# Kernel tuning notes

Hardware: AMD Instinct MI355X
Metric: run time of the kernel (lower is better)

## Reference

```python
import jax, jax.numpy as jnp
import numpy as np
import math

D_MODEL = 1024
NUM_HEADS = 16
HEAD_DIM = D_MODEL // NUM_HEADS
THETA = 10000.0
B, S = 2, 2048


def apply_rope(x, pos, theta=THETA):
    # x: [..., S, D]; pos: [S] int. Rotates consecutive (even, odd) pairs.
    d = x.shape[-1]
    inv_freq = theta ** (-jnp.arange(0, d, 2, dtype=jnp.float32) / d)  # [d/2]
    ang = pos.astype(jnp.float32)[:, None] * inv_freq[None, :]          # [S, d/2]
    cos, sin = jnp.cos(ang), jnp.sin(ang)
    xe = x[..., 0::2]
    xo = x[..., 1::2]
    re = xe * cos - xo * sin
    ro = xe * sin + xo * cos
    return jnp.stack([re, ro], axis=-1).reshape(x.shape)


def setup_inputs() -> dict:
    key = jax.random.key(0)
    ks = jax.random.split(key, 5)
    scale = 1.0 / math.sqrt(D_MODEL)
    return {
        "in_features": jax.random.normal(ks[0], (B, S, D_MODEL), dtype=jnp.float32),
        "token_positions": jnp.arange(S, dtype=jnp.int32),
        "wq": jax.random.normal(ks[1], (D_MODEL, D_MODEL), dtype=jnp.float32) * scale,
        "wk": jax.random.normal(ks[2], (D_MODEL, D_MODEL), dtype=jnp.float32) * scale,
        "wv": jax.random.normal(ks[3], (D_MODEL, D_MODEL), dtype=jnp.float32) * scale,
        "wo": jax.random.normal(ks[4], (D_MODEL, D_MODEL), dtype=jnp.float32) * scale,
    }


def reference(in_features, token_positions, wq, wk, wv, wo):
    x = in_features
    b, s, d = x.shape
    # Linear: y = x @ W.T  (weight stored as [out, in])
    def split_heads(y):
        return y.reshape(b, s, NUM_HEADS, HEAD_DIM).transpose(0, 2, 1, 3)  # [B,H,S,Dh]
    Q = split_heads(x @ wq.T)
    K = split_heads(x @ wk.T)
    V = split_heads(x @ wv.T)
    Q = apply_rope(Q, token_positions)
    K = apply_rope(K, token_positions)
    scores = jnp.einsum('bhqd,bhkd->bhqk', Q, K) / math.sqrt(HEAD_DIM)
    causal = jnp.tril(jnp.ones((s, s), dtype=bool))
    scores = jnp.where(causal, scores, -jnp.inf)
    weights = jax.nn.softmax(scores, axis=-1)
    out = jnp.einsum('bhqk,bhkd->bhqd', weights, V)  # [B,H,S,Dh]
    out = out.transpose(0, 2, 1, 3).reshape(b, s, d)
    return out @ wo.T
```

## Files before the change

kernel.cpp:

```cpp
#include <hip/hip_runtime.h>
#include <hip/hip_bf16.h>

typedef __bf16 bf16_t;
typedef __bf16 bf16x8 __attribute__((ext_vector_type(8)));
typedef __bf16 bf16x4 __attribute__((ext_vector_type(4)));
typedef float  f32x4  __attribute__((ext_vector_type(4)));
typedef float  f32x16 __attribute__((ext_vector_type(16)));
typedef unsigned int u32;
typedef unsigned int u32x2v __attribute__((ext_vector_type(2)));
typedef unsigned int u32x4v __attribute__((ext_vector_type(4)));

#define D_MODEL   1024
#define NQKV      3072
#define NUM_HEADS 16
#define HEAD_DIM  64
#define SEQ       2048
#define BATCH     2
#define NTOK      4096
#define SM_SCALE_LOG2E 0.18033688011112042f
#define NEG_BIG  (-3.0e38f)

__device__ __forceinline__ int swz128(int row, int bytecol) {
  return row*128 + ((((bytecol>>4) ^ (row&7))<<4) | (bytecol & 15));
}

__device__ __forceinline__ void gload16(const void* g, void* l) {
  __builtin_amdgcn_global_load_lds((const __attribute__((address_space(1))) u32*)g,
                                   (__attribute__((address_space(3))) u32*)l, 16, 0, 0);
}

__device__ __forceinline__ u32 cvtpk_bf16(float a, float b) {
  u32 r;
  asm("v_cvt_pk_bf16_f32 %0, %1, %2" : "=v"(r) : "v"(a), "v"(b));
  return r;
}

__device__ __forceinline__ void plswap(u32 &a, u32 &b) {
#if __has_builtin(__builtin_amdgcn_permlane32_swap)
  u32x2v r = __builtin_amdgcn_permlane32_swap(a, b, false, false);
  a = r[0]; b = r[1];
#else
  u32 xa = __shfl_xor((unsigned)a, 32, 64);
  u32 xb = __shfl_xor((unsigned)b, 32, 64);
  bool hi = (threadIdx.x & 32) != 0;
  a = hi ? xb : a;
  b = hi ? b : xa;
#endif
}

__device__ const unsigned char slot_order96[96] = {
  30,31,88,90,92,93,94,95,
  28,29,80,82,84,85,86,87,89,91,
  26,27,72,74,76,77,78,79,81,83,
  24,25,64,66,68,69,70,71,73,75,
  22,23,56,58,60,61,62,63,65,67,
  20,21,48,50,52,53,54,55,57,59,
  18,19,40,42,44,45,46,47,49,51,
  16,17,32,34,36,37,38,39,41,43,
  14,15,33,35,
  12,13, 10,11, 8,9, 6,7, 4,5, 2,3, 0,1
};

__global__ void cvt_x(const float* __restrict__ in, bf16_t* __restrict__ out) {
  int i = (blockIdx.x*256 + threadIdx.x)*4;
  float4 v = *reinterpret_cast<const float4*>(in + i);
  bf16x4 o; o[0]=(bf16_t)v.x; o[1]=(bf16_t)v.y; o[2]=(bf16_t)v.z; o[3]=(bf16_t)v.w;
  *reinterpret_cast<bf16x4*>(out + i) = o;
}

__global__ void cvt_w(const float* __restrict__ wq, const float* __restrict__ wk,
                      const float* __restrict__ wv, const float* __restrict__ wo,
                      bf16_t* __restrict__ wqkv, bf16_t* __restrict__ wob) {
  const int NW = D_MODEL*D_MODEL;
  int i = (blockIdx.x*256 + threadIdx.x)*4;
  float4 v;
  if      (i <   NW) v = *reinterpret_cast<const float4*>(wq + i);
  else if (i < 2*NW) v = *reinterpret_cast<const float4*>(wk + i - NW);
  else if (i < 3*NW) v = *reinterpret_cast<const float4*>(wv + i - 2*NW);
  else               v = *reinterpret_cast<const float4*>(wo + i - 3*NW);
  bf16x4 o; o[0]=(bf16_t)v.x; o[1]=(bf16_t)v.y; o[2]=(bf16_t)v.z; o[3]=(bf16_t)v.w;
  bf16_t* dst = (i < 3*NW) ? (wqkv + i) : (wob + i - 3*NW);
  *reinterpret_cast<bf16x4*>(dst) = o;
}

__global__ void rope_qk(bf16_t* __restrict__ QKV, const int* __restrict__ pos) {
  int i = blockIdx.x*256 + threadIdx.x;
  int j = i & 31;
  int hp = (i >> 5) & 15;
  int t  = i >> 9;
  float ang = (float)pos[t & (SEQ-1)] * exp2f(-(float)j * (13.287712379549449f/32.0f));
  float sv, cv; sincosf(ang, &sv, &cv);
  size_t base = (size_t)t*NQKV + hp*64 + 2*j;
  float xe = (float)QKV[base], xo = (float)QKV[base+1];
  QKV[base]   = (bf16_t)((xe*cv - xo*sv)*SM_SCALE_LOG2E);
  QKV[base+1] = (bf16_t)((xe*sv + xo*cv)*SM_SCALE_LOG2E);
  xe = (float)QKV[base+1024]; xo = (float)QKV[base+1025];
  QKV[base+1024] = (bf16_t)(xe*cv - xo*sv);
  QKV[base+1025] = (bf16_t)(xe*sv + xo*cv);
}

template<typename OutT, bool QKV>
__global__ __launch_bounds__(256, 1) void gemm8(const bf16_t* __restrict__ A,
                                                const bf16_t* __restrict__ B,
                                                OutT* __restrict__ C,
                                                bf16_t* __restrict__ Vt,
                                                int M, int N, int K) {
  __shared__ __align__(16) char lds[4][32768];
  int tid = threadIdx.x;
  int n0 = blockIdx.x*128, m0 = blockIdx.y*128;
  int wid = tid>>6, lane = tid&63;
  int wr = wid>>1, wc = wid&1;
  int lr = lane&15, lg = lane>>4;

  const int nT = K >> 6;

  int srow = tid >> 3;
  int sc8  = (tid & 7) ^ (srow & 7);
  const bf16_t* ga = A + (size_t)(m0 + srow)*K + sc8*8;
  const bf16_t* gb = B + (size_t)(n0 + srow)*K + sc8*8;

  f32x4 acc[4][4];
  #pragma unroll
  for (int a=0;a<4;a++)
    #pragma unroll
    for (int b=0;b<4;b++) acc[a][b] = (f32x4){0.f,0.f,0.f,0.f};

  auto stage = [&](int t) {
    char* s = lds[t&3];
    int k0 = t << 6;
    #pragma unroll
    for (int g=0; g<4; g++)
      gload16(ga + (size_t)(g*32)*K + k0, s + g*4096 + tid*16);
    #pragma unroll
    for (int g=0; g<4; g++)
      gload16(gb + (size_t)(g*32)*K + k0, s + 16384 + g*4096 + tid*16);
  };

  stage(0);
  if (nT > 1) stage(1);
  asm volatile("s_waitcnt vmcnt(8)" ::: "memory");
  __builtin_amdgcn_sched_barrier(0);
  __builtin_amdgcn_s_barrier();

  for (int t = 0; t < nT; ++t) {
    char* sA = lds[t&3];
    char* sB = sA + 16384;

    bf16x8 bq[4][2], aq[2][2];
    #pragma unroll
    for (int ni=0; ni<4; ni++)
      #pragma unroll
      for (int ks=0; ks<2; ks++)
        bq[ni][ks] = *reinterpret_cast<const bf16x8*>(sB + swz128(wc*64+ni*16+lr, ks*64+lg*16));
    #pragma unroll
    for (int mi=0; mi<2; mi++)
      #pragma unroll
      for (int ks=0; ks<2; ks++)
        aq[mi][ks] = *reinterpret_cast<const bf16x8*>(sA + swz128(wr*64+mi*16+lr, ks*64+lg*16));
    if (t + 2 < nT) stage(t + 2);
    asm volatile("s_waitcnt lgkmcnt(0)" ::: "memory");
    __builtin_amdgcn_sched_barrier(0);
    __builtin_amdgcn_s_setprio(1);
    #pragma unroll
    for (int mi=0; mi<2; mi++)
      #pragma unroll
      for (int ni=0; ni<4; ni++)
        #pragma unroll
        for (int ks=0; ks<2; ks++)
          acc[mi][ni] = __builtin_amdgcn_mfma_f32_16x16x32_bf16(aq[mi][ks], bq[ni][ks], acc[mi][ni], 0, 0, 0);
    __builtin_amdgcn_s_setprio(0);
    __builtin_amdgcn_s_barrier();

    bf16x8 aq2[2][2];
    #pragma unroll
    for (int mi=0; mi<2; mi++)
      #pragma unroll
      for (int ks=0; ks<2; ks++)
        aq2[mi][ks] = *reinterpret_cast<const bf16x8*>(sA + swz128(wr*64+(mi+2)*16+lr, ks*64+lg*16));
    asm volatile("s_waitcnt lgkmcnt(0)" ::: "memory");
    __builtin_amdgcn_sched_barrier(0);
    __builtin_amdgcn_s_setprio(1);
    #pragma unroll
    for (int mi=0; mi<2; mi++)
      #pragma unroll
      for (int ni=0; ni<4; ni++)
        #pragma unroll
        for (int ks=0; ks<2; ks++)
          acc[mi+2][ni] = __builtin_amdgcn_mfma_f32_16x16x32_bf16(aq2[mi][ks], bq[ni][ks], acc[mi+2][ni], 0, 0, 0);
    __builtin_amdgcn_s_setprio(0);
    if (t + 2 < nT)      { asm volatile("s_waitcnt vmcnt(8)" ::: "memory"); }
    else if (t + 1 < nT) { asm volatile("s_waitcnt vmcnt(0)" ::: "memory"); }
    __builtin_amdgcn_sched_barrier(0);
    __builtin_amdgcn_s_barrier();
  }

  if (!QKV || n0 < 2*D_MODEL) {
    #pragma unroll
    for (int mi=0;mi<4;mi++)
      #pragma unroll
      for (int ni=0;ni<4;ni++)
        #pragma unroll
        for (int r=0;r<4;r++) {
          int m = m0 + wr*64 + mi*16 + lg*4 + r;
          int n = n0 + wc*64 + ni*16 + lr;
          C[(size_t)m*N + n] = (OutT)acc[mi][ni][r];
        }
  } else {
    #pragma unroll
    for (int mi=0;mi<4;mi++)
      #pragma unroll
      for (int ni=0;ni<4;ni++)
        #pragma unroll
        for (int r=0;r<4;r++) {
          int m = m0 + wr*64 + mi*16 + lg*4 + r;
          int nl = n0 + wc*64 + ni*16 + lr - 2*D_MODEL;
          int h = nl >> 6, d = nl & 63;
          int bb = m >> 11, s = m & (SEQ-1);
          Vt[(((size_t)(bb*16 + h)*64 + d) << 11) + s] = (bf16_t)acc[mi][ni][r];
        }
  }
}

__global__ __launch_bounds__(64, 2) void attn7(const bf16_t* __restrict__ QKV,
                                               const bf16_t* __restrict__ Vt,
                                               bf16_t* __restrict__ pO,
                                               float2* __restrict__ pML) {
  __shared__ __align__(16) char sK[2][64*128];
  __shared__ __align__(16) char sV[64*128];

  int bh = blockIdx.x;
  int b = bh >> 4, h = bh & 15;
  int lane = threadIdx.x & 63;
  int q32 = lane & 31, hi = lane >> 5;
  int rsub = lane >> 3, sg = (lane & 7) ^ rsub;

  int s = slot_order96[blockIdx.y];
  int qw, t0, t1;
  if (s < 32) { qw = s; t0 = 0; t1 = (s >> 1) + 1; }
  else {
    int e = s - 32;
    qw = 32 + (e >> 1);
    int nt = (qw >> 1) + 1, h0 = (nt + 1) >> 1;
    t0 = (e & 1) ? h0 : 0;
    t1 = (e & 1) ? nt : h0;
  }
  int qt   = qw >> 1;
  int slot = bh*96 + s;
  int qg   = qw*32 + q32;

  bf16x8 qf[4];
  const bf16_t* qrow = QKV + (size_t)(b*SEQ + qw*32 + q32)*NQKV + h*64 + hi*8;
  #pragma unroll
  for (int d=0; d<4; d++) qf[d] = *reinterpret_cast<const bf16x8*>(qrow + d*16);

  const bf16_t* kgb = QKV + D_MODEL + ((size_t)(b*SEQ) + rsub)*NQKV + h*64 + sg*8;
  const bf16_t* vgb = Vt + (size_t)bh*64*SEQ + (size_t)rsub*SEQ + sg*8;

  auto stageK = [&](int t, int buf) {
    const bf16_t* src = kgb + (size_t)t*64*NQKV;
    #pragma unroll
    for (int c=0;c<8;c++)
      gload16(src + (size_t)(8*c)*NQKV, sK[buf] + c*1024 + lane*16);
  };
  auto stageV = [&](int t) {
    const bf16_t* src = vgb + t*64;
    #pragma unroll
    for (int c=0;c<8;c++)
      gload16(src + (size_t)(8*c)*SEQ, sV + c*1024 + lane*16);
  };

  f32x16 O0 = (f32x16)0.0f, O1 = (f32x16)0.0f;
  float mrun = NEG_BIG, lrun = 0.f;

  stageK(t0, 0); stageV(t0);
  if (t0 + 1 < t1) stageK(t0 + 1, 1);

  for (int ti = t0; ti < t1; ++ti) {
    int cur = (ti - t0) & 1;
    if (ti + 1 < t1) { asm volatile("s_waitcnt vmcnt(8)" ::: "memory"); }
    else             { asm volatile("s_waitcnt vmcnt(0)" ::: "memory"); }
    __builtin_amdgcn_sched_barrier(0);

    bf16x8 k0f[4], k1f[4];
    #pragma unroll
    for (int ds=0; ds<4; ds++) {
      k0f[ds] = *reinterpret_cast<const bf16x8*>(sK[cur] + swz128(q32,    ds*32 + hi*16));
      k1f[ds] = *reinterpret_cast<const bf16x8*>(sK[cur] + swz128(32+q32, ds*32 + hi*16));
    }
    f32x16 p0 = (f32x16)0.0f, p1 = (f32x16)0.0f;
    __builtin_amdgcn_s_setprio(1);
    #pragma unroll
    for (int ds=0; ds<4; ds++) {
      p0 = __builtin_amdgcn_mfma_f32_32x32x16_bf16(k0f[ds], qf[ds], p0, 0, 0, 0);
      p1 = __builtin_amdgcn_mfma_f32_32x32x16_bf16(k1f[ds], qf[ds], p1, 0, 0, 0);
    }
    __builtin_amdgcn_s_setprio(0);

    if (ti == qt) {
      #pragma unroll
      for (int r=0; r<16; r++) {
        int kg = ti*64 + (r&3) + 8*(r>>2) + 4*hi;
        if (kg      > qg) p0[r] = NEG_BIG;
        if (kg + 32 > qg) p1[r] = NEG_BIG;
      }
    }

    float mx[8];
    #pragma unroll
    for (int r=0;r<8;r++) mx[r] = fmaxf(fmaxf(p0[r],p0[r+8]), fmaxf(p1[r],p1[r+8]));
    #pragma unroll
    for (int st=4; st>0; st>>=1)
      #pragma unroll
      for (int r=0;r<st;r++) mx[r] = fmaxf(mx[r], mx[r+st]);
    float mt   = fmaxf(mx[0], __shfl_xor(mx[0], 32, 64));
    float mnew = fmaxf(mrun, mt);
    float alpha = exp2f(mrun - mnew);
    #pragma unroll
    for (int r=0; r<16; r++) {
      p0[r] = exp2f(p0[r] - mnew);
      p1[r] = exp2f(p1[r] - mnew);
    }
    float sx[8];
    #pragma unroll
    for (int r=0;r<8;r++) sx[r] = (p0[r]+p0[r+8]) + (p1[r]+p1[r+8]);
    #pragma unroll
    for (int st=4; st>0; st>>=1)
      #pragma unroll
      for (int r=0;r<st;r++) sx[r] += sx[r+st];
    float stot = sx[0] + __shfl_xor(sx[0], 32, 64);
    lrun = lrun*alpha + stot;
    mrun = mnew;
    O0 *= alpha; O1 *= alpha;

    u32 pk0[8], pk1[8];
    #pragma unroll
    for (int i2=0; i2<8; i2++) {
      pk0[i2] = cvtpk_bf16(p0[2*i2], p0[2*i2+1]);
      pk1[i2] = cvtpk_bf16(p1[2*i2], p1[2*i2+1]);
    }
    plswap(pk0[0], pk0[2]); plswap(pk0[1], pk0[3]);
    plswap(pk0[4], pk0[6]); plswap(pk0[5], pk0[7]);
    plswap(pk1[0], pk1[2]); plswap(pk1[1], pk1[3]);
    plswap(pk1[4], pk1[6]); plswap(pk1[5], pk1[7]);

    bf16x8 pa[4];
    pa[0] = __builtin_bit_cast(bf16x8, (u32x4v){pk0[0],pk0[1],pk0[2],pk0[3]});
    pa[1] = __builtin_bit_cast(bf16x8, (u32x4v){pk0[4],pk0[5],pk0[6],pk0[7]});
    pa[2] = __builtin_bit_cast(bf16x8, (u32x4v){pk1[0],pk1[1],pk1[2],pk1[3]});
    pa[3] = __builtin_bit_cast(bf16x8, (u32x4v){pk1[4],pk1[5],pk1[6],pk1[7]});

    bf16x8 v0f[4], v1f[4];
    #pragma unroll
    for (int ks=0; ks<4; ks++) {
      v0f[ks] = *reinterpret_cast<const bf16x8*>(sV + swz128(q32,    ks*32 + hi*16));
      v1f[ks] = *reinterpret_cast<const bf16x8*>(sV + swz128(32+q32, ks*32 + hi*16));
    }
    asm volatile("s_waitcnt lgkmcnt(0)" ::: "memory");
    __builtin_amdgcn_sched_barrier(0);
    if (ti + 1 < t1) stageV(ti + 1);
    if (ti + 2 < t1) stageK(ti + 2, cur);

    __builtin_amdgcn_s_setprio(1);
    #pragma unroll
    for (int ks=0; ks<4; ks++) {
      O0 = __builtin_amdgcn_mfma_f32_32x32x16_bf16(v0f[ks], pa[ks], O0, 0, 0, 0);
      O1 = __builtin_amdgcn_mfma_f32_32x32x16_bf16(v1f[ks], pa[ks], O1, 0, 0, 0);
    }
    __builtin_amdgcn_s_setprio(0);
  }

  bf16_t* prow = pO + ((size_t)slot*2048 + q32*64);
  #pragma unroll
  for (int rg=0; rg<4; rg++) {
    int d0 = 8*rg + 4*hi;
    u32 a0 = cvtpk_bf16(O0[4*rg],   O0[4*rg+1]);
    u32 a1 = cvtpk_bf16(O0[4*rg+2], O0[4*rg+3]);
    *reinterpret_cast<u32x2v*>(prow + d0) = (u32x2v){a0, a1};
    u32 b0 = cvtpk_bf16(O1[4*rg],   O1[4*rg+1]);
    u32 b1 = cvtpk_bf16(O1[4*rg+2], O1[4*rg+3]);
    *reinterpret_cast<u32x2v*>(prow + 32 + d0) = (u32x2v){b0, b1};
  }
  if (hi == 0)
    pML[slot*32 + q32] = make_float2(mrun, lrun);
}

__global__ __launch_bounds__(128) void combine(const bf16_t* __restrict__ pO,
                                               const float2* __restrict__ pML,
                                               bf16_t* __restrict__ Of) {
  int qw = blockIdx.x, bh = blockIdx.y;
  int b = bh >> 4, h = bh & 15;
  int t = threadIdx.x;
  int q = t >> 2, d0 = (t & 3) * 16;
  bf16x8 r0, r1;
  if (qw < 32) {
    int slot = bh*96 + qw;
    float2 ml = pML[slot*32 + q];
    float inv = 1.0f / ml.y;
    const bf16x8* src = reinterpret_cast<const bf16x8*>(pO + (size_t)slot*2048 + q*64 + d0);
    bf16x8 o0 = src[0], o1 = src[1];
    #pragma unroll
    for (int i=0;i<8;i++) {
      r0[i] = (bf16_t)((float)o0[i]*inv);
      r1[i] = (bf16_t)((float)o1[i]*inv);
    }
  } else {
    int s0 = bh*96 + 32 + (qw-32)*2;
    float2 mlA = pML[s0*32 + q];
    float2 mlB = pML[(s0+1)*32 + q];
    float m  = fmaxf(mlA.x, mlB.x);
    float a0 = exp2f(mlA.x - m), a1 = exp2f(mlB.x - m);
    float inv = 1.0f / (a0*mlA.y + a1*mlB.y);
    a0 *= inv; a1 *= inv;
    const bf16x8* sA = reinterpret_cast<const bf16x8*>(pO + (size_t)s0*2048 + q*64 + d0);
    const bf16x8* sB = reinterpret_cast<const bf16x8*>(pO + (size_t)(s0+1)*2048 + q*64 + d0);
    bf16x8 oa0 = sA[0], oa1 = sA[1], ob0 = sB[0], ob1 = sB[1];
    #pragma unroll
    for (int i=0;i<8;i++) {
      r0[i] = (bf16_t)(a0*(float)oa0[i] + a1*(float)ob0[i]);
      r1[i] = (bf16_t)(a0*(float)oa1[i] + a1*(float)ob1[i]);
    }
  }
  bf16x8* dst = reinterpret_cast<bf16x8*>(Of + ((size_t)(b*SEQ) + qw*32 + q)*D_MODEL + h*64 + d0);
  dst[0] = r0; dst[1] = r1;
}

extern "C" void kernel_launch(void* const* d_in, const int* in_sizes, int n_in,
                              void* d_out, int out_size, void* d_ws, size_t ws_size,
                              hipStream_t stream) {
  const float* x   = (const float*)d_in[0];
  const int*   pos = (const int*)  d_in[1];
  const float* wq  = (const float*)d_in[2];
  const float* wk  = (const float*)d_in[3];
  const float* wv  = (const float*)d_in[4];
  const float* wo  = (const float*)d_in[5];
  float* out = (float*)d_out;

  char* ws = (char*)d_ws;
  bf16_t* xb   = (bf16_t*)(ws);
  bf16_t* wqkv = (bf16_t*)(ws + ( 8u<<20));
  bf16_t* wob  = (bf16_t*)(ws + (14u<<20));
  bf16_t* QKV  = (bf16_t*)(ws + (16u<<20));
  bf16_t* Vtb  = (bf16_t*)(ws + (40u<<20));
  bf16_t* pO   = (bf16_t*)(ws);
  float2* pML  = (float2*)(ws + (13u<<20));
  bf16_t* Of   = (bf16_t*)(ws + (40u<<20));

  cvt_x<<<NTOK*D_MODEL/1024, 256, 0, stream>>>(x, xb);
  cvt_w<<<4*D_MODEL*D_MODEL/1024, 256, 0, stream>>>(wq, wk, wv, wo, wqkv, wob);

  dim3 gqkv(NQKV/128, NTOK/128);
  gemm8<bf16_t, true><<<gqkv, 256, 0, stream>>>(xb, wqkv, QKV, Vtb, NTOK, NQKV, D_MODEL);

  rope_qk<<<NTOK*NUM_HEADS*32/256, 256, 0, stream>>>(QKV, pos);

  dim3 gattn(32, 96);
  attn7<<<gattn, 64, 0, stream>>>(QKV, Vtb, pO, pML);

  dim3 gcomb(64, 32);
  combine<<<gcomb, 128, 0, stream>>>(pO, pML, Of);

  dim3 gout(D_MODEL/128, NTOK/128);
  gemm8<float, false><<<gout, 256, 0, stream>>>(Of, wob, out, nullptr, NTOK, D_MODEL, D_MODEL);
}
```

Before: 135.3 us.

## Single-buffer K/V in attention, loading all fragments upfront and prefetching next tile

The attention kernel drops the double-buffered K shared-memory tile and uses one K and one V buffer. Each iteration now reads all K and V fragments into registers at the start, then issues the global loads for the next tile so they overlap with the QK^T, softmax and PV work. A full vmcnt(0) wait at the end of each iteration replaces the staggered waits. This halves K LDS usage, which could raise occupancy, but holds more fragments in registers and shortens how far ahead the prefetch runs.

```diff
diff --git a/kernel.cpp b/kernel.cpp
--- a/kernel.cpp
+++ b/kernel.cpp
@@ -221,11 +221,11 @@
   }
 }
 
-__global__ __launch_bounds__(64, 2) void attn7(const bf16_t* __restrict__ QKV,
+__global__ __launch_bounds__(64, 2) void attn9(const bf16_t* __restrict__ QKV,
                                                const bf16_t* __restrict__ Vt,
                                                bf16_t* __restrict__ pO,
                                                float2* __restrict__ pML) {
-  __shared__ __align__(16) char sK[2][64*128];
+  __shared__ __align__(16) char sK[64*128];
   __shared__ __align__(16) char sV[64*128];
 
   int bh = blockIdx.x;
@@ -256,11 +256,11 @@
   const bf16_t* kgb = QKV + D_MODEL + ((size_t)(b*SEQ) + rsub)*NQKV + h*64 + sg*8;
   const bf16_t* vgb = Vt + (size_t)bh*64*SEQ + (size_t)rsub*SEQ + sg*8;
 
-  auto stageK = [&](int t, int buf) {
+  auto stageK = [&](int t) {
     const bf16_t* src = kgb + (size_t)t*64*NQKV;
     #pragma unroll
     for (int c=0;c<8;c++)
-      gload16(src + (size_t)(8*c)*NQKV, sK[buf] + c*1024 + lane*16);
+      gload16(src + (size_t)(8*c)*NQKV, sK + c*1024 + lane*16);
   };
   auto stageV = [&](int t) {
     const bf16_t* src = vgb + t*64;
@@ -272,21 +272,23 @@
   f32x16 O0 = (f32x16)0.0f, O1 = (f32x16)0.0f;
   float mrun = NEG_BIG, lrun = 0.f;
 
-  stageK(t0, 0); stageV(t0);
-  if (t0 + 1 < t1) stageK(t0 + 1, 1);
+  stageK(t0); stageV(t0);
+  asm volatile("s_waitcnt vmcnt(0)" ::: "memory");
+  __builtin_amdgcn_sched_barrier(0);
 
   for (int ti = t0; ti < t1; ++ti) {
-    int cur = (ti - t0) & 1;
-    if (ti + 1 < t1) { asm volatile("s_waitcnt vmcnt(8)" ::: "memory"); }
-    else             { asm volatile("s_waitcnt vmcnt(0)" ::: "memory"); }
+    bf16x8 k0f[4], k1f[4], v0f[4], v1f[4];
+    #pragma unroll
+    for (int ds=0; ds<4; ds++) {
+      k0f[ds] = *reinterpret_cast<const bf16x8*>(sK + swz128(q32,    ds*32 + hi*16));
+      k1f[ds] = *reinterpret_cast<const bf16x8*>(sK + swz128(32+q32, ds*32 + hi*16));
+      v0f[ds] = *reinterpret_cast<const bf16x8*>(sV + swz128(q32,    ds*32 + hi*16));
+      v1f[ds] = *reinterpret_cast<const bf16x8*>(sV + swz128(32+q32, ds*32 + hi*16));
+    }
+    asm volatile("s_waitcnt lgkmcnt(0)" ::: "memory");
     __builtin_amdgcn_sched_barrier(0);
-
-    bf16x8 k0f[4], k1f[4];
-    #pragma unroll
-    for (int ds=0; ds<4; ds++) {
-      k0f[ds] = *reinterpret_cast<const bf16x8*>(sK[cur] + swz128(q32,    ds*32 + hi*16));
-      k1f[ds] = *reinterpret_cast<const bf16x8*>(sK[cur] + swz128(32+q32, ds*32 + hi*16));
-    }
+    if (ti + 1 < t1) { stageK(ti + 1); stageV(ti + 1); }
+
     f32x16 p0 = (f32x16)0.0f, p1 = (f32x16)0.0f;
     __builtin_amdgcn_s_setprio(1);
     #pragma unroll
@@ -349,17 +351,6 @@
     pa[2] = __builtin_bit_cast(bf16x8, (u32x4v){pk1[0],pk1[1],pk1[2],pk1[3]});
     pa[3] = __builtin_bit_cast(bf16x8, (u32x4v){pk1[4],pk1[5],pk1[6],pk1[7]});
 
-    bf16x8 v0f[4], v1f[4];
-    #pragma unroll
-    for (int ks=0; ks<4; ks++) {
-      v0f[ks] = *reinterpret_cast<const bf16x8*>(sV + swz128(q32,    ks*32 + hi*16));
-      v1f[ks] = *reinterpret_cast<const bf16x8*>(sV + swz128(32+q32, ks*32 + hi*16));
-    }
-    asm volatile("s_waitcnt lgkmcnt(0)" ::: "memory");
-    __builtin_amdgcn_sched_barrier(0);
-    if (ti + 1 < t1) stageV(ti + 1);
-    if (ti + 2 < t1) stageK(ti + 2, cur);
-
     __builtin_amdgcn_s_setprio(1);
     #pragma unroll
     for (int ks=0; ks<4; ks++) {
@@ -367,6 +358,11 @@
       O1 = __builtin_amdgcn_mfma_f32_32x32x16_bf16(v1f[ks], pa[ks], O1, 0, 0, 0);
     }
     __builtin_amdgcn_s_setprio(0);
+
+    if (ti + 1 < t1) {
+      asm volatile("s_waitcnt vmcnt(0)" ::: "memory");
+      __builtin_amdgcn_sched_barrier(0);
+    }
   }
 
   bf16_t* prow = pO + ((size_t)slot*2048 + q32*64);
@@ -454,7 +450,7 @@
   rope_qk<<<NTOK*NUM_HEADS*32/256, 256, 0, stream>>>(QKV, pos);
 
   dim3 gattn(32, 96);
-  attn7<<<gattn, 64, 0, stream>>>(QKV, Vtb, pO, pML);
+  attn9<<<gattn, 64, 0, stream>>>(QKV, Vtb, pO, pML);
 
   dim3 gcomb(64, 32);
   combine<<<gcomb, 128, 0, stream>>>(pO, pML, Of);
```

Measured after the change: 131.3 us. 1.03x faster.
